# Performance work log

Hardware: AMD Instinct MI355X
Metric: run time of the kernel (lower is better)

The kernel has to match this reference:

```python
import jax, jax.numpy as jnp
import numpy as np

IN_SIZE = 784
Z_DIM = 128
K_DIM = 8192
BATCH = 16384
ENC_HIDDEN = [512, 256]          # EncoderMLP default
DEC_SIZES = [Z_DIM, 256, 512, 784]  # DecoderMLP default: [latent, *hidden]


def _linear(x, w, b):
    return x @ w + b


def find_nearest(query, target):
    # Faithful to: sqrt(sum((Q-T)^2, -1)).min(1)[1]; sqrt is monotone so
    # argmin of squared distance is identical. Computed via the GEMM
    # expansion instead of materializing the (N,K,D) broadcast tensor.
    q2 = jnp.sum(query * query, axis=1, keepdims=True)        # [N,1]
    t2 = jnp.sum(target * target, axis=1)                     # [K]
    d2 = q2 - 2.0 * (query @ target.T) + t2[None, :]          # [N,K]
    idx = jnp.argmin(d2, axis=1)
    return target[idx]


def setup_inputs() -> dict:
    key = jax.random.key(0)
    ks = jax.random.split(key, 16)
    s = 0.02
    inp = {"X": jax.random.uniform(ks[0], (BATCH, 1, 28, 28), dtype=jnp.float32)}
    # Encoder: 784 -> 512 -> 256 (mlp blocks, ReLU) -> 128 (plain Linear)
    enc_sizes = [IN_SIZE] + ENC_HIDDEN + [Z_DIM]
    for i, (din, dout) in enumerate(zip(enc_sizes, enc_sizes[1:]), 1):
        inp[f"enc_w{i}"] = s * jax.random.normal(ks[i], (din, dout), dtype=jnp.float32)
        inp[f"enc_b{i}"] = jnp.zeros((dout,), dtype=jnp.float32)
    # Codebook
    inp["codebook"] = jax.random.normal(ks[8], (K_DIM, Z_DIM), dtype=jnp.float32)
    # Decoder: 128 -> 256 -> 512 -> 784 (mlp blocks, ReLU) + sigmoid out
    for i, (din, dout) in enumerate(zip(DEC_SIZES, DEC_SIZES[1:]), 1):
        inp[f"dec_w{i}"] = s * jax.random.normal(ks[8 + i], (din, dout), dtype=jnp.float32)
        inp[f"dec_b{i}"] = jnp.zeros((dout,), dtype=jnp.float32)
    return inp


def reference(X, enc_w1, enc_b1, enc_w2, enc_b2, enc_w3, enc_b3, codebook,
              dec_w1, dec_b1, dec_w2, dec_b2, dec_w3, dec_b3):
    x = X.reshape(-1, IN_SIZE)
    # Encoder (mlp_block = Linear+ReLU, final layer plain Linear)
    h = jax.nn.relu(_linear(x, enc_w1, enc_b1))
    h = jax.nn.relu(_linear(h, enc_w2, enc_b2))
    z_enc = _linear(h, enc_w3, enc_b3)                         # [N, Z]
    # Nearest codebook vector for each encoding
    z_dec = find_nearest(z_enc, codebook)                      # [N, Z]
    # Decoder
    d = jax.nn.relu(_linear(z_dec, dec_w1, dec_b1))
    d = jax.nn.relu(_linear(d, dec_w2, dec_b2))
    d = jax.nn.relu(_linear(d, dec_w3, dec_b3))
    x_recon = jax.nn.sigmoid(d).reshape(-1, 1, 28, 28)
    # Nearest encoding for each codebook vector (for embedding loss)
    z_enc_for_embd = find_nearest(codebook, z_enc)             # [K, Z]
    return (x_recon, z_enc, z_dec, z_enc_for_embd)
```

## Files before the change

kernel.cpp:

```cpp
#include <hip/hip_runtime.h>
#include <math.h>

using u16 = unsigned short;
using u32 = unsigned int;
using u64 = unsigned long long;

typedef __bf16 bf16x8 __attribute__((ext_vector_type(8)));
typedef short  s16x8  __attribute__((ext_vector_type(8)));
typedef float  f32x4  __attribute__((ext_vector_type(4)));

__device__ __forceinline__ float b2f(u16 u){
  union { u32 i; float f; } x; x.i = ((u32)u) << 16; return x.f;
}
__device__ __forceinline__ u16 f2b(float f){
  union { float f; u32 i; } x; x.f = f;
  u32 i = x.i;
  u32 r = (i + 0x7fffu + ((i >> 16) & 1u)) >> 16;
  return (u16)r;
}
__device__ __forceinline__ f32x4 mfma16(s16x8 a, s16x8 b, f32x4 c){
  return __builtin_amdgcn_mfma_f32_16x16x32_bf16(
      __builtin_bit_cast(bf16x8, a), __builtin_bit_cast(bf16x8, b), c, 0, 0, 0);
}
__device__ __forceinline__ u64 shfl_xor_u64(u64 v, int m){
  int lo = __shfl_xor((int)(u32)v, m);
  int hi = __shfl_xor((int)(u32)(v >> 32), m);
  return ((u64)(u32)hi << 32) | (u32)lo;
}
__device__ __forceinline__ u64 umin64(u64 a, u64 b){ return a < b ? a : b; }
__device__ __forceinline__ u64 packmin(float v, int idx){
  u32 b = __float_as_uint(v);
  b = (b & 0x80000000u) ? ~b : (b | 0x80000000u);
  return ((u64)b << 32) | (u32)idx;
}
__device__ __forceinline__ void gload16(const void* g, void* l){
  __builtin_amdgcn_global_load_lds(
      (const __attribute__((address_space(1))) unsigned int*)g,
      (__attribute__((address_space(3))) unsigned int*)l, 16, 0, 0);
}

__global__ __launch_bounds__(256) void canary_k(float* out, float code){
  out[threadIdx.x] = code;
}

__global__ __launch_bounds__(256) void prep_weights(
    const float* __restrict__ w1, const float* __restrict__ w2, const float* __restrict__ w3,
    const float* __restrict__ dw1, const float* __restrict__ dw2, const float* __restrict__ dw3,
    const float* __restrict__ cb,
    u16* __restrict__ o1h, u16* __restrict__ o1l, u16* __restrict__ o2h, u16* __restrict__ o2l,
    u16* __restrict__ o3h, u16* __restrict__ o3l, u16* __restrict__ o4h, u16* __restrict__ o4l,
    u16* __restrict__ o5h, u16* __restrict__ o5l, u16* __restrict__ o6h, u16* __restrict__ o6l,
    u16* __restrict__ cbh, u16* __restrict__ cbl)
{
  const int bid = blockIdx.x, tid = threadIdx.x;
  if (bid >= 288){
    size_t e4 = ((size_t)(bid - 288) * 256 + tid) * 4;
    float4 v = *(const float4*)(cb + e4);
    ushort4 h, l;
    h.x = f2b(v.x); l.x = f2b(v.x - b2f(h.x));
    h.y = f2b(v.y); l.y = f2b(v.y - b2f(h.y));
    h.z = f2b(v.z); l.z = f2b(v.z - b2f(h.z));
    h.w = f2b(v.w); l.w = f2b(v.w - b2f(h.w));
    *(ushort4*)(cbh + e4) = h;
    *(ushort4*)(cbl + e4) = l;
    return;
  }
  __shared__ float ldsT[64][65];
  const float* src; u16 *hi, *lo; int K, N, Kp, kpT; int base;
  if      (bid < 104){ src=w1;  hi=o1h; lo=o1l; K=784; N=512; Kp=832; kpT=13; base=0;   }
  else if (bid < 136){ src=w2;  hi=o2h; lo=o2l; K=512; N=256; Kp=512; kpT=8;  base=104; }
  else if (bid < 144){ src=w3;  hi=o3h; lo=o3l; K=256; N=128; Kp=256; kpT=4;  base=136; }
  else if (bid < 152){ src=dw1; hi=o4h; lo=o4l; K=128; N=256; Kp=128; kpT=2;  base=144; }
  else if (bid < 184){ src=dw2; hi=o5h; lo=o5l; K=256; N=512; Kp=256; kpT=4;  base=152; }
  else               { src=dw3; hi=o6h; lo=o6l; K=512; N=784; Kp=512; kpT=8;  base=184; }
  int b = bid - base;
  int kp0 = (b % kpT) * 64, n0 = (b / kpT) * 64;
  const int cc = tid & 63, g = tid >> 6;
  #pragma unroll
  for (int r = 0; r < 16; r++){
    int rr = g * 16 + r;
    int kp = kp0 + rr, n = n0 + cc;
    float v = 0.f;
    if (kp < K && n < N) v = src[(size_t)kp * N + n];
    ldsT[cc][rr] = v;
  }
  __syncthreads();
  #pragma unroll
  for (int w2_ = 0; w2_ < 16; w2_++){
    int nn = g * 16 + w2_;
    int n = n0 + nn, kp = kp0 + cc;
    if (n < N){
      float v = ldsT[nn][cc];
      u16 h = f2b(v);
      size_t e = (size_t)n * Kp + kp;
      hi[e] = h;
      lo[e] = f2b(v - b2f(h));
    }
  }
}

__device__ __forceinline__ void norm_row(const float* __restrict__ src, float* __restrict__ dst){
  const float4* r = (const float4*)src;
  float s = 0.f;
  for (int k = 0; k < 32; k++){
    float4 p = r[k];
    s += p.x * p.x + p.y * p.y + p.z * p.z + p.w * p.w;
  }
  *dst = s;
}

struct __align__(16) SmemGemm {
  u16 Ah[128][72];
  u16 Al[128][72];
  u16 Bh[128][72];
  u16 Bl[128][72];
};

template<int ACT, int OUTP>
__device__ __forceinline__ void gemm_body(
    SmemGemm& sm,
    const float* __restrict__ A, const u16* __restrict__ B0, const u16* __restrict__ B1,
    const float* __restrict__ bias, float* __restrict__ Cf,
    u16* __restrict__ P0, u16* __restrict__ P1,
    int Astr, int KLIM, int Kp, int KT, int N, int nRowsB, int bx, int by)
{
  const int tid = threadIdx.x;
  const int m0 = by * 128, n0 = bx * 128;
  const int wave = tid >> 6, lane = tid & 63;
  const int wm = (wave >> 1) * 64, wn = (wave & 1) * 64;
  const int quad = lane >> 4, l15 = lane & 15;
  f32x4 acc[4][4] = {};

  for (int kt = 0; kt < KT; ++kt){
    const int kb = kt * 64;
    #pragma unroll
    for (int c = 0; c < 8; c++){
      int idx = c * 256 + tid;
      int r = idx >> 4, c4 = (idx & 15) * 4;
      float4 v = make_float4(0.f, 0.f, 0.f, 0.f);
      if (kb + c4 < KLIM)
        v = *(const float4*)(A + (size_t)(m0 + r) * Astr + kb + c4);
      ushort4 h, l;
      h.x = f2b(v.x); l.x = f2b(v.x - b2f(h.x));
      h.y = f2b(v.y); l.y = f2b(v.y - b2f(h.y));
      h.z = f2b(v.z); l.z = f2b(v.z - b2f(h.z));
      h.w = f2b(v.w); l.w = f2b(v.w - b2f(h.w));
      *(ushort4*)&sm.Ah[r][c4] = h;
      *(ushort4*)&sm.Al[r][c4] = l;
    }
    #pragma unroll
    for (int c = 0; c < 4; c++){
      int idx = c * 256 + tid;
      int r = idx >> 3, col = (idx & 7) * 8;
      int rb = n0 + r; rb = rb < nRowsB ? rb : nRowsB - 1;
      *(uint4*)&sm.Bh[r][col] = *(const uint4*)(B0 + (size_t)rb * Kp + kb + col);
      *(uint4*)&sm.Bl[r][col] = *(const uint4*)(B1 + (size_t)rb * Kp + kb + col);
    }
    __syncthreads();
    #pragma unroll
    for (int kh = 0; kh < 2; ++kh){
      s16x8 ah[4], al[4], bh[4], bl[4];
      #pragma unroll
      for (int t4 = 0; t4 < 4; t4++){
        ah[t4] = *(const s16x8*)&sm.Ah[wm + t4 * 16 + l15][kh * 32 + quad * 8];
        al[t4] = *(const s16x8*)&sm.Al[wm + t4 * 16 + l15][kh * 32 + quad * 8];
        bh[t4] = *(const s16x8*)&sm.Bh[wn + t4 * 16 + l15][kh * 32 + quad * 8];
        bl[t4] = *(const s16x8*)&sm.Bl[wn + t4 * 16 + l15][kh * 32 + quad * 8];
      }
      #pragma unroll
      for (int mt = 0; mt < 4; mt++)
        #pragma unroll
        for (int nt = 0; nt < 4; nt++){
          acc[mt][nt] = mfma16(ah[mt], bh[nt], acc[mt][nt]);
          acc[mt][nt] = mfma16(ah[mt], bl[nt], acc[mt][nt]);
          acc[mt][nt] = mfma16(al[mt], bh[nt], acc[mt][nt]);
        }
    }
    __syncthreads();
  }

  float bvs[4]; int cols[4];
  #pragma unroll
  for (int nt = 0; nt < 4; nt++){
    int cN = n0 + wn + nt * 16 + l15;
    cols[nt] = cN;
    int cc = cN < N ? cN : N - 1;
    bvs[nt] = bias[cc];
  }
  #pragma unroll
  for (int mt = 0; mt < 4; mt++){
    int rbase = m0 + wm + mt * 16 + quad * 4;
    #pragma unroll
    for (int nt = 0; nt < 4; nt++){
      if (cols[nt] < N){
        #pragma unroll
        for (int r = 0; r < 4; r++){
          float v = acc[mt][nt][r] + bvs[nt];
          if (ACT >= 1) v = v > 0.f ? v : 0.f;
          if (ACT == 2) v = 1.f / (1.f + expf(-v));
          size_t off = (size_t)(rbase + r) * N + cols[nt];
          if (OUTP == 2){
            P0[off] = f2b(v);
          } else {
            Cf[off] = v;
            if (OUTP == 1){
              u16 h = f2b(v);
              P0[off] = h;
              P1[off] = f2b(v - b2f(h));
            }
          }
        }
      }
    }
  }
}

template<int ACT, int OUTP>
__global__ __launch_bounds__(256, 2) void gemm_k(
    const float* __restrict__ A, const u16* __restrict__ B0, const u16* __restrict__ B1,
    const float* __restrict__ bias, float* __restrict__ Cf,
    u16* __restrict__ P0, u16* __restrict__ P1,
    int Astr, int KLIM, int Kp, int KT, int N, int nRowsB)
{
  __shared__ SmemGemm sm;
  gemm_body<ACT, OUTP>(sm, A, B0, B1, bias, Cf, P0, P1, Astr, KLIM, Kp, KT, N, nRowsB,
                       blockIdx.x, blockIdx.y);
}

__global__ __launch_bounds__(256, 2) void fused1(
    const float* __restrict__ X,  const u16* __restrict__ W1h, const u16* __restrict__ W1l,
    const float* __restrict__ b1, float* __restrict__ h1,
    const float* __restrict__ cb, const u16* __restrict__ D1h, const u16* __restrict__ D1l,
    const float* __restrict__ db1, float* __restrict__ g1, float* __restrict__ t2f)
{
  __shared__ SmemGemm sm;
  int bid = blockIdx.x;
  if (bid < 512){
    gemm_body<1,0>(sm, X, W1h, W1l, b1, h1, nullptr, nullptr, 784, 784, 832, 13, 512, 512,
                   bid & 3, bid >> 2);
  } else if (bid < 640){
    int b = bid - 512;
    gemm_body<1,0>(sm, cb, D1h, D1l, db1, g1, nullptr, nullptr, 128, 128, 128, 2, 256, 256,
                   b & 1, b >> 1);
  } else {
    int r = (bid - 640) * 256 + threadIdx.x;
    norm_row(cb + (size_t)r * 128, t2f + r);
  }
}

__global__ __launch_bounds__(256, 2) void fused3(
    const float* __restrict__ h2, const u16* __restrict__ W3h, const u16* __restrict__ W3l,
    const float* __restrict__ b3, float* __restrict__ zenc,
    u16* __restrict__ zhi, u16* __restrict__ zlo,
    const float* __restrict__ g1, const u16* __restrict__ D2h, const u16* __restrict__ D2l,
    const float* __restrict__ db2, float* __restrict__ g2)
{
  __shared__ SmemGemm sm;
  int bid = blockIdx.x;
  if (bid < 128){
    gemm_body<0,1>(sm, h2, W3h, W3l, b3, zenc, zhi, zlo, 256, 256, 256, 4, 128, 128,
                   0, bid);
  } else {
    int b = bid - 128;
    gemm_body<1,0>(sm, g1, D2h, D2l, db2, g2, nullptr, nullptr, 256, 256, 256, 4, 512, 512,
                   b & 3, b >> 2);
  }
}

struct __align__(16) DistSmem {
  u16 smem[2][16384];
  u64 colbuf[4][128];
  u64 sRow[2][128];
  float q2s[128];
};

__device__ __forceinline__ void dist_body(
    DistSmem& sm,
    const u16* __restrict__ Zh, const u16* __restrict__ Zl,
    const u16* __restrict__ Bh, const u16* __restrict__ Bl,
    const float* __restrict__ zenc, const float* __restrict__ t2,
    u64* __restrict__ rowp, u64* __restrict__ colp, int strip, int iblk)
{
  const int tid = threadIdx.x;
  const int i0 = iblk * 128;
  const int wave = tid >> 6, lane = tid & 63;
  const int wm = (wave >> 1) * 32, wn = (wave & 1) * 64;
  const int quad = lane >> 4, l15 = lane & 15;

  const int swz = (l15 & 7) << 4;
  const int cof0 = (((quad << 4)     ) ^ swz) >> 1;
  const int cof1 = (((quad << 4) | 64) ^ swz) >> 1;

  if (tid < 128){
    norm_row(zenc + (size_t)(i0 + tid) * 128, &sm.q2s[tid]);
  }

  s16x8 zh[2][2][2], zl[2][2][2];
  #pragma unroll
  for (int kb = 0; kb < 2; kb++)
    #pragma unroll
    for (int kh = 0; kh < 2; kh++)
      #pragma unroll
      for (int mt = 0; mt < 2; mt++){
        size_t off = (size_t)(i0 + wm + mt * 16 + l15) * 128 + kb * 64 + kh * 32 + quad * 8;
        zh[kb][kh][mt] = *(const s16x8*)(Zh + off);
        zl[kb][kh][mt] = *(const s16x8*)(Zl + off);
      }

  #define STAGE(jt_, kb_, buf_) {                                              \
    size_t jb = (size_t)(strip * 2048 + (jt_) * 128) * 128 + (kb_) * 64;       \
    _Pragma("unroll")                                                          \
    for (int c = 0; c < 2; c++){                                               \
      int ci = c * 512 + tid;                                                  \
      int row = ci >> 3;                                                       \
      size_t g = jb + (size_t)row * 128 + (size_t)(((ci & 7) ^ (row & 7)) * 8);\
      u16* lp = &sm.smem[buf_][ci * 8];                                        \
      gload16(Bh + g, lp);                                                     \
      gload16(Bl + g, lp + 8192);                                              \
    }                                                                          \
  }

  #define COMPUTE(buf_, kb_) {                                                 \
    __builtin_amdgcn_s_setprio(1);                                             \
    _Pragma("unroll")                                                          \
    for (int kh = 0; kh < 2; kh++){                                            \
      const int cof = kh ? cof1 : cof0;                                        \
      s16x8 bh[4], bl[4];                                                      \
      _Pragma("unroll")                                                        \
      for (int nt = 0; nt < 4; nt++){                                          \
        int off = (wn + nt * 16 + l15) * 64 + cof;                             \
        bh[nt] = *(const s16x8*)&sm.smem[buf_][off];                           \
        bl[nt] = *(const s16x8*)&sm.smem[buf_][8192 + off];                    \
      }                                                                        \
      _Pragma("unroll")                                                        \
      for (int mt = 0; mt < 2; mt++)                                           \
        _Pragma("unroll")                                                      \
        for (int nt = 0; nt < 4; nt++){                                        \
          acc[mt][nt] = mfma16(zh[kb_][kh][mt], bh[nt], acc[mt][nt]);          \
          acc[mt][nt] = mfma16(zh[kb_][kh][mt], bl[nt], acc[mt][nt]);          \
          acc[mt][nt] = mfma16(zl[kb_][kh][mt], bh[nt], acc[mt][nt]);          \
          acc[mt][nt] = mfma16(zl[kb_][kh][mt], bl[nt], acc[mt][nt]);          \
        }                                                                      \
    }                                                                          \
    __builtin_amdgcn_s_setprio(0);                                             \
  }

  STAGE(0, 0, 0);

  asm volatile("s_waitcnt lgkmcnt(0)" ::: "memory");
  __builtin_amdgcn_s_barrier();

  float qv[2][4];
  #pragma unroll
  for (int mt = 0; mt < 2; mt++)
    #pragma unroll
    for (int r = 0; r < 4; r++)
      qv[mt][r] = sm.q2s[wm + mt * 16 + quad * 4 + r];

  u64 rowm[2][4];
  #pragma unroll
  for (int mt = 0; mt < 2; mt++)
    #pragma unroll
    for (int r = 0; r < 4; r++) rowm[mt][r] = ~0ULL;

  #pragma unroll 1
  for (int jt = 0; jt < 16; ++jt){
    const int j0 = strip * 2048 + jt * 128;
    float t2v[4]; int gj[4];
    #pragma unroll
    for (int nt = 0; nt < 4; nt++){
      gj[nt] = j0 + wn + nt * 16 + l15;
      t2v[nt] = t2[gj[nt]];
    }
    f32x4 acc[2][4] = {};

    STAGE(jt, 1, 1);
    asm volatile("s_waitcnt vmcnt(8)" ::: "memory");
    __builtin_amdgcn_s_barrier();
    COMPUTE(0, 0)
    __builtin_amdgcn_s_barrier();
    if (jt < 15){
      STAGE(jt + 1, 0, 0);
      asm volatile("s_waitcnt vmcnt(4)" ::: "memory");
    } else {
      asm volatile("s_waitcnt vmcnt(0)" ::: "memory");
    }
    __builtin_amdgcn_s_barrier();
    COMPUTE(1, 1)

    #pragma unroll
    for (int mt = 0; mt < 2; mt++){
      #pragma unroll
      for (int r = 0; r < 4; r++){
        float qq = qv[mt][r];
        float rbest = (qq - 2.f * acc[mt][0][r]) + t2v[0];
        int   ridx  = gj[0];
        #pragma unroll
        for (int nt = 1; nt < 4; nt++){
          float v = (qq - 2.f * acc[mt][nt][r]) + t2v[nt];
          if (v < rbest){ rbest = v; ridx = gj[nt]; }
        }
        rowm[mt][r] = umin64(rowm[mt][r], packmin(rbest, ridx));
      }
    }
    #pragma unroll
    for (int nt = 0; nt < 4; nt++){
      float cbest = 3.4e38f; int cidx = 0;
      #pragma unroll
      for (int mt = 0; mt < 2; mt++){
        #pragma unroll
        for (int r = 0; r < 4; r++){
          float vc = (t2v[nt] - 2.f * acc[mt][nt][r]) + qv[mt][r];
          if (vc < cbest){ cbest = vc; cidx = i0 + wm + mt * 16 + quad * 4 + r; }
        }
      }
      u64 p = packmin(cbest, cidx);
      p = umin64(p, shfl_xor_u64(p, 16));
      p = umin64(p, shfl_xor_u64(p, 32));
      if (quad == 0)
        sm.colbuf[wave >> 1][wn + nt * 16 + l15] = p;
    }
    __builtin_amdgcn_s_barrier();
    if (tid < 128){
      u64 p = umin64(umin64(sm.colbuf[0][tid], sm.colbuf[1][tid]),
                     umin64(sm.colbuf[2][tid], sm.colbuf[3][tid]));
      colp[(size_t)iblk * 8192 + j0 + tid] = p;
    }
  }
  #undef STAGE
  #undef COMPUTE

  #pragma unroll
  for (int mt = 0; mt < 2; mt++)
    #pragma unroll
    for (int r = 0; r < 4; r++){
      u64 p = rowm[mt][r];
      p = umin64(p, shfl_xor_u64(p, 1));
      p = umin64(p, shfl_xor_u64(p, 2));
      p = umin64(p, shfl_xor_u64(p, 4));
      p = umin64(p, shfl_xor_u64(p, 8));
      rowm[mt][r] = p;
    }
  if (l15 == 0){
    #pragma unroll
    for (int mt = 0; mt < 2; mt++)
      #pragma unroll
      for (int r = 0; r < 4; r++)
        sm.sRow[wave & 1][wm + mt * 16 + quad * 4 + r] = rowm[mt][r];
  }
  __syncthreads();
  if (tid < 128)
    rowp[(size_t)strip * 16384 + i0 + tid] = umin64(sm.sRow[0][tid], sm.sRow[1][tid]);
}

__global__ __launch_bounds__(512, 2) void dist_k(
    const u16* __restrict__ Zh, const u16* __restrict__ Zl,
    const u16* __restrict__ Bh, const u16* __restrict__ Bl,
    const float* __restrict__ zenc, const float* __restrict__ t2,
    u64* __restrict__ rowp, u64* __restrict__ colp)
{
  __shared__ DistSmem sm;
  dist_body(sm, Zh, Zl, Bh, Bl, zenc, t2, rowp, colp, blockIdx.x & 3, blockIdx.x >> 2);
}

union SmemF5 {
  SmemGemm g;
  struct { u64 s[4][64]; int sidx[64]; } r;
};

__global__ __launch_bounds__(256, 2) void fused5(
    const float* __restrict__ g2, const u16* __restrict__ D3h, const u16* __restrict__ D3l,
    const float* __restrict__ db3, u16* __restrict__ xdecb,
    const u64* __restrict__ rowp, const u64* __restrict__ colp,
    const float* __restrict__ cb, const float* __restrict__ zenc,
    float* __restrict__ zdec, float* __restrict__ zembd, int* __restrict__ rowidx)
{
  __shared__ SmemF5 sm;
  int bid = blockIdx.x;
  if (bid < 448){
    gemm_body<2,2>(sm.g, g2, D3h, D3l, db3, nullptr, xdecb, nullptr,
                   512, 512, 512, 8, 784, 784, bid % 7, bid / 7);
    return;
  }
  bid -= 448;
  int tid = threadIdx.x;
  if (bid < 256){
    int base = bid * 64;
    int n = base + (tid & 63);
    u64 best = ~0ULL;
    for (int p = tid >> 6; p < 4; p += 4)
      best = umin64(best, rowp[(size_t)p * 16384 + n]);
    sm.r.s[tid >> 6][tid & 63] = best;
    __syncthreads();
    if (tid < 64){
      u64 b = umin64(umin64(sm.r.s[0][tid], sm.r.s[1][tid]),
                     umin64(sm.r.s[2][tid], sm.r.s[3][tid]));
      int idx = (int)(b & 0xffffffffULL);
      idx = idx < 0 ? 0 : (idx > 8191 ? 8191 : idx);
      sm.r.sidx[tid] = idx;
      rowidx[base + tid] = idx;
    }
    __syncthreads();
    for (int q = 0; q < 32; q++){
      int e = q * 256 + tid; int r = e >> 7, c = e & 127;
      zdec[(size_t)(base + r) * 128 + c] = cb[(size_t)sm.r.sidx[r] * 128 + c];
    }
  } else {
    int base = (bid - 256) * 64;
    int n = base + (tid & 63);
    u64 best = ~0ULL;
    for (int p = tid >> 6; p < 128; p += 4)
      best = umin64(best, colp[(size_t)p * 8192 + n]);
    sm.r.s[tid >> 6][tid & 63] = best;
    __syncthreads();
    if (tid < 64){
      u64 b = umin64(umin64(sm.r.s[0][tid], sm.r.s[1][tid]),
                     umin64(sm.r.s[2][tid], sm.r.s[3][tid]));
      int idx = (int)(b & 0xffffffffULL);
      idx = idx < 0 ? 0 : (idx > 16383 ? 16383 : idx);
      sm.r.sidx[tid] = idx;
    }
    __syncthreads();
    for (int q = 0; q < 32; q++){
      int e = q * 256 + tid; int r = e >> 7, c = e & 127;
      zembd[(size_t)(base + r) * 128 + c] = zenc[(size_t)sm.r.sidx[r] * 128 + c];
    }
  }
}

__global__ __launch_bounds__(256) void gather_xrec(
    const u16* __restrict__ xdecb, const int* __restrict__ rowidx, float* __restrict__ xrec)
{
  size_t q = (size_t)blockIdx.x * 256 + threadIdx.x;
  int row = (int)(q / 196), c4 = (int)(q % 196) * 4;
  int idx = rowidx[row];
  idx = idx < 0 ? 0 : (idx > 8191 ? 8191 : idx);
  ushort4 v = *(const ushort4*)(xdecb + (size_t)idx * 784 + c4);
  float4 o = make_float4(b2f(v.x), b2f(v.y), b2f(v.z), b2f(v.w));
  *(float4*)(xrec + (size_t)row * 784 + c4) = o;
}

extern "C" void kernel_launch(void* const* d_in, const int* in_sizes, int n_in,
                              void* d_out, int out_size, void* d_ws, size_t ws_size,
                              hipStream_t stream){
  const float* X   = (const float*)d_in[0];
  const float* w1  = (const float*)d_in[1];  const float* b1  = (const float*)d_in[2];
  const float* w2  = (const float*)d_in[3];  const float* b2  = (const float*)d_in[4];
  const float* w3  = (const float*)d_in[5];  const float* b3  = (const float*)d_in[6];
  const float* cb  = (const float*)d_in[7];
  const float* dw1 = (const float*)d_in[8];  const float* db1 = (const float*)d_in[9];
  const float* dw2 = (const float*)d_in[10]; const float* db2 = (const float*)d_in[11];
  const float* dw3 = (const float*)d_in[12]; const float* db3 = (const float*)d_in[13];

  float* out   = (float*)d_out;
  float* xrec  = out;
  float* zenc  = out + 12845056;
  float* zdec  = zenc + 2097152;
  float* zembd = zdec + 2097152;

  const size_t NEEDED = 22020096;
  if (ws_size < NEEDED){
    canary_k<<<1, 256, 0, stream>>>(out, 1000.0f + (float)(ws_size >> 20));
    return;
  }

  char* ob = (char*)d_out;
  float* h1   = (float*)(ob + 0);
  u16*   zhi  = (u16*)(ob + 8388608);
  u16*   zlo  = (u16*)(ob + 12582912);
  float* g2   = (float*)(ob + 16777216);
  float* g1   = (float*)(ob + 33554432);
  u16*   cbhi = (u16*)(ob + 41943040);
  u16*   cblo = (u16*)(ob + 44040192);
  u64*   colp = (u64*)(ob + 0);

  char* w = (char*)d_ws;
  u16* W1Th = (u16*)(w + 0);        u16* W1Tl = (u16*)(w + 851968);
  u16* W2Th = (u16*)(w + 1703936);  u16* W2Tl = (u16*)(w + 1966080);
  u16* W3Th = (u16*)(w + 2228224);  u16* W3Tl = (u16*)(w + 2293760);
  u16* D1Th = (u16*)(w + 2359296);  u16* D1Tl = (u16*)(w + 2424832);
  u16* D2Th = (u16*)(w + 2490368);  u16* D2Tl = (u16*)(w + 2752512);
  u16* D3Th = (u16*)(w + 3014656);  u16* D3Tl = (u16*)(w + 3817472);
  float* t2f = (float*)(w + 4620288);
  int*  rowi = (int*)(w + 4653056);
  u64*  rowp = (u64*)(w + 4718592);
  float* h2  = (float*)(w + 5242880);
  u16* xdecb = (u16*)(w + 5242880);

  prep_weights<<<1312, 256, 0, stream>>>(w1, w2, w3, dw1, dw2, dw3, cb,
      W1Th, W1Tl, W2Th, W2Tl, W3Th, W3Tl, D1Th, D1Tl, D2Th, D2Tl, D3Th, D3Tl, cbhi, cblo);

  fused1<<<672, 256, 0, stream>>>(X, W1Th, W1Tl, b1, h1, cb, D1Th, D1Tl, db1, g1, t2f);

  gemm_k<1, 0><<<dim3(2, 128), 256, 0, stream>>>(h1, W2Th, W2Tl, b2, h2, nullptr, nullptr,
                                                 512, 512, 512, 8, 256, 256);

  fused3<<<384, 256, 0, stream>>>(h2, W3Th, W3Tl, b3, zenc, zhi, zlo,
                                  g1, D2Th, D2Tl, db2, g2);

  dist_k<<<512, 512, 0, stream>>>(zhi, zlo, cbhi, cblo, zenc, t2f, rowp, colp);

  fused5<<<832, 256, 0, stream>>>(g2, D3Th, D3Tl, db3, xdecb,
                                  rowp, colp, cb, zenc, zdec, zembd, rowi);

  gather_xrec<<<12544, 256, 0, stream>>>(xdecb, rowi, xrec);
}
```

Before: 476.8 us.

## Load codebook fragments directly from global and reduce column minima with atomicMin

The distance kernel no longer stages codebook hi/lo tiles through double-buffered LDS with async global-to-LDS loads. Each wave now reads its B fragments straight from global memory into registers. Column-wise argmin partials are no longer written per row-block and reduced later: each wave does an atomicMin into an 8192-entry array, which an extra block in fused3 initializes. This removes LDS traffic, barriers and the 128-way partial reduction pass, but every B fragment is now fetched redundantly by the four waves sharing it and it adds global atomics.

Result: slower. 588.0 us (+23.3%).

```diff
diff --git a/kernel.cpp b/kernel.cpp
--- a/kernel.cpp
+++ b/kernel.cpp
@@ -32,11 +32,6 @@
   u32 b = __float_as_uint(v);
   b = (b & 0x80000000u) ? ~b : (b | 0x80000000u);
   return ((u64)b << 32) | (u32)idx;
-}
-__device__ __forceinline__ void gload16(const void* g, void* l){
-  __builtin_amdgcn_global_load_lds(
-      (const __attribute__((address_space(1))) unsigned int*)g,
-      (__attribute__((address_space(3))) unsigned int*)l, 16, 0, 0);
 }
 
 __global__ __launch_bounds__(256) void canary_k(float* out, float code){
@@ -253,23 +248,24 @@
     const float* __restrict__ b3, float* __restrict__ zenc,
     u16* __restrict__ zhi, u16* __restrict__ zlo,
     const float* __restrict__ g1, const u16* __restrict__ D2h, const u16* __restrict__ D2l,
-    const float* __restrict__ db2, float* __restrict__ g2)
+    const float* __restrict__ db2, float* __restrict__ g2, u64* __restrict__ colp)
 {
   __shared__ SmemGemm sm;
   int bid = blockIdx.x;
   if (bid < 128){
     gemm_body<0,1>(sm, h2, W3h, W3l, b3, zenc, zhi, zlo, 256, 256, 256, 4, 128, 128,
                    0, bid);
-  } else {
+  } else if (bid < 384){
     int b = bid - 128;
     gemm_body<1,0>(sm, g1, D2h, D2l, db2, g2, nullptr, nullptr, 256, 256, 256, 4, 512, 512,
                    b & 3, b >> 2);
+  } else {
+    for (int q = 0; q < 32; q++)
+      colp[q * 256 + threadIdx.x] = ~0ULL;
   }
 }
 
 struct __align__(16) DistSmem {
-  u16 smem[2][16384];
-  u64 colbuf[4][128];
   u64 sRow[2][128];
   float q2s[128];
 };
@@ -287,10 +283,6 @@
   const int wm = (wave >> 1) * 32, wn = (wave & 1) * 64;
   const int quad = lane >> 4, l15 = lane & 15;
 
-  const int swz = (l15 & 7) << 4;
-  const int cof0 = (((quad << 4)     ) ^ swz) >> 1;
-  const int cof1 = (((quad << 4) | 64) ^ swz) >> 1;
-
   if (tid < 128){
     norm_row(zenc + (size_t)(i0 + tid) * 128, &sm.q2s[tid]);
   }
@@ -307,48 +299,7 @@
         zl[kb][kh][mt] = *(const s16x8*)(Zl + off);
       }
 
-  #define STAGE(jt_, kb_, buf_) {                                              \
-    size_t jb = (size_t)(strip * 2048 + (jt_) * 128) * 128 + (kb_) * 64;       \
-    _Pragma("unroll")                                                          \
-    for (int c = 0; c < 2; c++){                                               \
-      int ci = c * 512 + tid;                                                  \
-      int row = ci >> 3;                                                       \
-      size_t g = jb + (size_t)row * 128 + (size_t)(((ci & 7) ^ (row & 7)) * 8);\
-      u16* lp = &sm.smem[buf_][ci * 8];                                        \
-      gload16(Bh + g, lp);                                                     \
-      gload16(Bl + g, lp + 8192);                                              \
-    }                                                                          \
-  }
-
-  #define COMPUTE(buf_, kb_) {                                                 \
-    __builtin_amdgcn_s_setprio(1);                                             \
-    _Pragma("unroll")                                                          \
-    for (int kh = 0; kh < 2; kh++){                                            \
-      const int cof = kh ? cof1 : cof0;                                        \
-      s16x8 bh[4], bl[4];                                                      \
-      _Pragma("unroll")                                                        \
-      for (int nt = 0; nt < 4; nt++){                                          \
-        int off = (wn + nt * 16 + l15) * 64 + cof;                             \
-        bh[nt] = *(const s16x8*)&sm.smem[buf_][off];                           \
-        bl[nt] = *(const s16x8*)&sm.smem[buf_][8192 + off];                    \
-      }                                                                        \
-      _Pragma("unroll")                                                        \
-      for (int mt = 0; mt < 2; mt++)                                           \
-        _Pragma("unroll")                                                      \
-        for (int nt = 0; nt < 4; nt++){                                        \
-          acc[mt][nt] = mfma16(zh[kb_][kh][mt], bh[nt], acc[mt][nt]);          \
-          acc[mt][nt] = mfma16(zh[kb_][kh][mt], bl[nt], acc[mt][nt]);          \
-          acc[mt][nt] = mfma16(zl[kb_][kh][mt], bh[nt], acc[mt][nt]);          \
-          acc[mt][nt] = mfma16(zl[kb_][kh][mt], bl[nt], acc[mt][nt]);          \
-        }                                                                      \
-    }                                                                          \
-    __builtin_amdgcn_s_setprio(0);                                             \
-  }
-
-  STAGE(0, 0, 0);
-
-  asm volatile("s_waitcnt lgkmcnt(0)" ::: "memory");
-  __builtin_amdgcn_s_barrier();
+  __syncthreads();
 
   float qv[2][4];
   #pragma unroll
@@ -374,19 +325,29 @@
     }
     f32x4 acc[2][4] = {};
 
-    STAGE(jt, 1, 1);
-    asm volatile("s_waitcnt vmcnt(8)" ::: "memory");
-    __builtin_amdgcn_s_barrier();
-    COMPUTE(0, 0)
-    __builtin_amdgcn_s_barrier();
-    if (jt < 15){
-      STAGE(jt + 1, 0, 0);
-      asm volatile("s_waitcnt vmcnt(4)" ::: "memory");
-    } else {
-      asm volatile("s_waitcnt vmcnt(0)" ::: "memory");
-    }
-    __builtin_amdgcn_s_barrier();
-    COMPUTE(1, 1)
+    #pragma unroll
+    for (int kb = 0; kb < 2; kb++)
+      #pragma unroll
+      for (int kh = 0; kh < 2; kh++){
+        s16x8 bh[4], bl[4];
+        #pragma unroll
+        for (int nt = 0; nt < 4; nt++){
+          size_t off = (size_t)(j0 + wn + nt * 16 + l15) * 128 + kb * 64 + kh * 32 + quad * 8;
+          bh[nt] = *(const s16x8*)(Bh + off);
+          bl[nt] = *(const s16x8*)(Bl + off);
+        }
+        __builtin_amdgcn_s_setprio(1);
+        #pragma unroll
+        for (int mt = 0; mt < 2; mt++)
+          #pragma unroll
+          for (int nt = 0; nt < 4; nt++){
+            acc[mt][nt] = mfma16(zh[kb][kh][mt], bh[nt], acc[mt][nt]);
+            acc[mt][nt] = mfma16(zh[kb][kh][mt], bl[nt], acc[mt][nt]);
+            acc[mt][nt] = mfma16(zl[kb][kh][mt], bh[nt], acc[mt][nt]);
+            acc[mt][nt] = mfma16(zl[kb][kh][mt], bl[nt], acc[mt][nt]);
+          }
+        __builtin_amdgcn_s_setprio(0);
+      }
 
     #pragma unroll
     for (int mt = 0; mt < 2; mt++){
@@ -418,17 +379,9 @@
       p = umin64(p, shfl_xor_u64(p, 16));
       p = umin64(p, shfl_xor_u64(p, 32));
       if (quad == 0)
-        sm.colbuf[wave >> 1][wn + nt * 16 + l15] = p;
-    }
-    __builtin_amdgcn_s_barrier();
-    if (tid < 128){
-      u64 p = umin64(umin64(sm.colbuf[0][tid], sm.colbuf[1][tid]),
-                     umin64(sm.colbuf[2][tid], sm.colbuf[3][tid]));
-      colp[(size_t)iblk * 8192 + j0 + tid] = p;
-    }
-  }
-  #undef STAGE
-  #undef COMPUTE
+        atomicMin(colp + gj[nt], p);
+    }
+  }
 
   #pragma unroll
   for (int mt = 0; mt < 2; mt++)
@@ -507,15 +460,8 @@
     }
   } else {
     int base = (bid - 256) * 64;
-    int n = base + (tid & 63);
-    u64 best = ~0ULL;
-    for (int p = tid >> 6; p < 128; p += 4)
-      best = umin64(best, colp[(size_t)p * 8192 + n]);
-    sm.r.s[tid >> 6][tid & 63] = best;
-    __syncthreads();
     if (tid < 64){
-      u64 b = umin64(umin64(sm.r.s[0][tid], sm.r.s[1][tid]),
-                     umin64(sm.r.s[2][tid], sm.r.s[3][tid]));
+      u64 b = colp[base + tid];
       int idx = (int)(b & 0xffffffffULL);
       idx = idx < 0 ? 0 : (idx > 16383 ? 16383 : idx);
       sm.r.sidx[tid] = idx;
@@ -566,13 +512,13 @@
 
   char* ob = (char*)d_out;
   float* h1   = (float*)(ob + 0);
+  u64*   colp = (u64*)(ob + 0);
   u16*   zhi  = (u16*)(ob + 8388608);
   u16*   zlo  = (u16*)(ob + 12582912);
   float* g2   = (float*)(ob + 16777216);
   float* g1   = (float*)(ob + 33554432);
   u16*   cbhi = (u16*)(ob + 41943040);
   u16*   cblo = (u16*)(ob + 44040192);
-  u64*   colp = (u64*)(ob + 0);
 
   char* w = (char*)d_ws;
   u16* W1Th = (u16*)(w + 0);        u16* W1Tl = (u16*)(w + 851968);
@@ -595,8 +541,8 @@
   gemm_k<1, 0><<<dim3(2, 128), 256, 0, stream>>>(h1, W2Th, W2Tl, b2, h2, nullptr, nullptr,
                                                  512, 512, 512, 8, 256, 256);
 
-  fused3<<<384, 256, 0, stream>>>(h2, W3Th, W3Tl, b3, zenc, zhi, zlo,
-                                  g1, D2Th, D2Tl, db2, g2);
+  fused3<<<385, 256, 0, stream>>>(h2, W3Th, W3Tl, b3, zenc, zhi, zlo,
+                                  g1, D2Th, D2Tl, db2, g2, colp);
 
   dist_k<<<512, 512, 0, stream>>>(zhi, zlo, cbhi, cblo, zenc, t2f, rowp, colp);
 
```
